# Performance work log

Hardware: AMD Instinct MI355X
Metric: run time of the kernel (lower is better)

## Reference

```python
import jax, jax.numpy as jnp
import numpy as np

HIDDEN = 1024
VOCAB = 128000

def setup_inputs() -> dict:
    key = jax.random.key(0)
    ks = jax.random.split(key, 9)
    s = 0.02
    return {
        "seq_input": jax.random.randint(ks[0], (1,), 0, VOCAB),
        "hidden": jax.random.normal(ks[1], (1, 1, HIDDEN), dtype=jnp.float32),
        "emb": jax.random.normal(ks[2], (VOCAB, HIDDEN), dtype=jnp.float32) * s,
        "w_ih": jax.random.normal(ks[3], (3 * HIDDEN, HIDDEN), dtype=jnp.float32) * s,
        "w_hh": jax.random.normal(ks[4], (3 * HIDDEN, HIDDEN), dtype=jnp.float32) * s,
        "b_ih": jax.random.normal(ks[5], (3 * HIDDEN,), dtype=jnp.float32) * s,
        "b_hh": jax.random.normal(ks[6], (3 * HIDDEN,), dtype=jnp.float32) * s,
        "w_out": jax.random.normal(ks[7], (VOCAB, HIDDEN), dtype=jnp.float32) * s,
        "b_out": jax.random.normal(ks[8], (VOCAB,), dtype=jnp.float32) * s,
    }

def reference(seq_input, hidden, emb, w_ih, w_hh, b_ih, b_hh, w_out, b_out):
    # embedding lookup + relu: [1, H]
    x = jax.nn.relu(emb[seq_input])
    h = hidden[0]  # [1, H] (num_layers=1, batch=1)
    # single-step GRU (PyTorch gate ordering: r, z, n)
    gi = x @ w_ih.T + b_ih     # [1, 3H]
    gh = h @ w_hh.T + b_hh     # [1, 3H]
    i_r, i_z, i_n = jnp.split(gi, 3, axis=-1)
    h_r, h_z, h_n = jnp.split(gh, 3, axis=-1)
    r = jax.nn.sigmoid(i_r + h_r)
    z = jax.nn.sigmoid(i_z + h_z)
    n = jnp.tanh(i_n + r * h_n)
    h_new = (1.0 - z) * n + z * h  # [1, H]
    # output projection + log-softmax over vocab: [1, V]
    logits = h_new @ w_out.T + b_out
    logprobs = jax.nn.log_softmax(logits, axis=1)
    return logprobs, h_new[None]  # hidden back to [1,1,H]
```

## Files before the change

### kernel.cpp

```cpp
#include <hip/hip_runtime.h>

#define H 1024
#define V 128000

#define WS_GI   0
#define WS_GH   3072
#define WS_HN   6144
#define WS_PART 7168
#define WS_FIN  7424

__device__ __forceinline__ float wave_sum(float acc) {
    #pragma unroll
    for (int m = 32; m >= 1; m >>= 1) acc += __shfl_xor(acc, m);
    return acc;
}

__global__ void gates_kernel(const int* __restrict__ seq,
                             const float* __restrict__ hidden,
                             const float* __restrict__ emb,
                             const float* __restrict__ w_ih,
                             const float* __restrict__ w_hh,
                             const float* __restrict__ b_ih,
                             const float* __restrict__ b_hh,
                             float* __restrict__ ws) {
    const int wid  = threadIdx.x >> 6;
    const int lane = threadIdx.x & 63;
    const int row  = blockIdx.x * 4 + wid;
    if (row >= 6144) return;
    const int idx = seq[0];

    const float* wrow;
    const float* v;
    float bias;
    bool relu_in;
    if (row < 3072) {
        wrow = w_ih + (size_t)row * H;
        v    = emb + (size_t)idx * H;
        bias = b_ih[row];
        relu_in = true;
    } else {
        const int r = row - 3072;
        wrow = w_hh + (size_t)r * H;
        v    = hidden;
        bias = b_hh[r];
        relu_in = false;
    }

    float acc = 0.f;
    #pragma unroll
    for (int k = 0; k < 4; ++k) {
        const int j = lane * 4 + k * 256;
        float4 wv = *(const float4*)(wrow + j);
        float4 vv = *(const float4*)(v + j);
        if (relu_in) {
            vv.x = fmaxf(vv.x, 0.f); vv.y = fmaxf(vv.y, 0.f);
            vv.z = fmaxf(vv.z, 0.f); vv.w = fmaxf(vv.w, 0.f);
        }
        acc += wv.x * vv.x + wv.y * vv.y + wv.z * vv.z + wv.w * vv.w;
    }
    acc = wave_sum(acc);
    if (lane == 0) ws[row] = acc + bias;
}

__global__ void gru_kernel(const float* __restrict__ hidden,
                           float* __restrict__ ws,
                           float* __restrict__ out) {
    const int i = threadIdx.x;
    const float gi_r = ws[WS_GI + i];
    const float gi_z = ws[WS_GI + H + i];
    const float gi_n = ws[WS_GI + 2 * H + i];
    const float gh_r = ws[WS_GH + i];
    const float gh_z = ws[WS_GH + H + i];
    const float gh_n = ws[WS_GH + 2 * H + i];
    const float r = 1.f / (1.f + expf(-(gi_r + gh_r)));
    const float z = 1.f / (1.f + expf(-(gi_z + gh_z)));
    const float n = tanhf(gi_n + r * gh_n);
    const float h = hidden[i];
    const float hn = (1.f - z) * n + z * h;
    ws[WS_HN + i] = hn;
    out[V + i] = hn;
}

__global__ void logits_kernel(const float* __restrict__ w_out,
                              const float* __restrict__ b_out,
                              const float* __restrict__ ws,
                              float* __restrict__ out) {
    const int wid  = threadIdx.x >> 6;
    const int lane = threadIdx.x & 63;
    const float* h = ws + WS_HN;
    float4 hv[4];
    #pragma unroll
    for (int k = 0; k < 4; ++k) hv[k] = *(const float4*)(h + lane * 4 + k * 256);

    const int nwaves = gridDim.x * 4;
    for (int row = blockIdx.x * 4 + wid; row < V; row += nwaves) {
        const float* wr = w_out + (size_t)row * H;
        float acc = 0.f;
        #pragma unroll
        for (int k = 0; k < 4; ++k) {
            float4 wv = *(const float4*)(wr + lane * 4 + k * 256);
            acc += wv.x * hv[k].x + wv.y * hv[k].y + wv.z * hv[k].z + wv.w * hv[k].w;
        }
        acc = wave_sum(acc);
        if (lane == 0) out[row] = acc + b_out[row];
    }
}

__device__ __forceinline__ void online_combine(float& m, float& s, float om, float os) {
    const float M = fmaxf(m, om);
    s = s * expf(m - M) + os * expf(om - M);
    m = M;
}

__global__ void smax_partial(const float* __restrict__ out, float* __restrict__ ws) {
    const int base = blockIdx.x * 1024 + threadIdx.x;
    float m = -1e30f, s = 0.f;
    #pragma unroll
    for (int k = 0; k < 4; ++k) {
        const float x = out[base + k * 256];
        if (x > m) { s = s * expf(m - x) + 1.f; m = x; }
        else       { s += expf(x - m); }
    }
    #pragma unroll
    for (int d = 1; d < 64; d <<= 1) {
        const float om = __shfl_xor(m, d);
        const float os = __shfl_xor(s, d);
        online_combine(m, s, om, os);
    }
    __shared__ float sm[4], sss[4];
    const int wid  = threadIdx.x >> 6;
    const int lane = threadIdx.x & 63;
    if (lane == 0) { sm[wid] = m; sss[wid] = s; }
    __syncthreads();
    if (threadIdx.x == 0) {
        float M = sm[0], S = sss[0];
        #pragma unroll
        for (int w = 1; w < 4; ++w) online_combine(M, S, sm[w], sss[w]);
        ws[WS_PART + 2 * blockIdx.x]     = M;
        ws[WS_PART + 2 * blockIdx.x + 1] = S;
    }
}

__global__ void smax_final(float* __restrict__ ws) {
    const int lane = threadIdx.x;
    float m = -1e30f, s = 0.f;
    for (int i = lane; i < 125; i += 64) {
        online_combine(m, s, ws[WS_PART + 2 * i], ws[WS_PART + 2 * i + 1]);
    }
    #pragma unroll
    for (int d = 1; d < 64; d <<= 1) {
        const float om = __shfl_xor(m, d);
        const float os = __shfl_xor(s, d);
        online_combine(m, s, om, os);
    }
    if (lane == 0) { ws[WS_FIN] = m; ws[WS_FIN + 1] = logf(s); }
}

__global__ void smax_write(float* __restrict__ out, const float* __restrict__ ws) {
    const float c = ws[WS_FIN] + ws[WS_FIN + 1];
    const int i = (blockIdx.x * 256 + threadIdx.x) * 4;
    float4 v = *(float4*)(out + i);
    v.x -= c; v.y -= c; v.z -= c; v.w -= c;
    *(float4*)(out + i) = v;
}

extern "C" void kernel_launch(void* const* d_in, const int* in_sizes, int n_in,
                              void* d_out, int out_size, void* d_ws, size_t ws_size,
                              hipStream_t stream) {
    const int*   seq    = (const int*)d_in[0];
    const float* hidden = (const float*)d_in[1];
    const float* emb    = (const float*)d_in[2];
    const float* w_ih   = (const float*)d_in[3];
    const float* w_hh   = (const float*)d_in[4];
    const float* b_ih   = (const float*)d_in[5];
    const float* b_hh   = (const float*)d_in[6];
    const float* w_out  = (const float*)d_in[7];
    const float* b_out  = (const float*)d_in[8];
    float* out = (float*)d_out;
    float* ws  = (float*)d_ws;

    gates_kernel<<<1536, 256, 0, stream>>>(seq, hidden, emb, w_ih, w_hh, b_ih, b_hh, ws);
    gru_kernel<<<1, 1024, 0, stream>>>(hidden, ws, out);
    logits_kernel<<<2000, 256, 0, stream>>>(w_out, b_out, ws, out);
    smax_partial<<<125, 256, 0, stream>>>(out, ws);
    smax_final<<<1, 64, 0, stream>>>(ws);
    smax_write<<<125, 256, 0, stream>>>(out, ws);
}
```

Before: 115.7 us.

## Fuse GRU cell and softmax partials into logits kernel, cut launches to three

Each logits block now recomputes the GRU cell update redundantly into shared memory, replacing the single-block gru kernel. The online max/sum-exp is accumulated inside the logits loop, which removes the separate partial-reduction pass over the logits. The final reduction over 2000 partials is folded into each block of the write kernel. This removes three launches and one read of the vocab-sized logits, at the cost of redundant gate work per block and each write block re-reducing all 2000 partials.

Measured after the change: 111.6 us. 1.04x faster.

```diff
diff --git a/kernel.cpp b/kernel.cpp
--- a/kernel.cpp
+++ b/kernel.cpp
@@ -2,17 +2,22 @@
 
 #define H 1024
 #define V 128000
+#define NBLK_LOGITS 2000
 
 #define WS_GI   0
 #define WS_GH   3072
-#define WS_HN   6144
-#define WS_PART 7168
-#define WS_FIN  7424
+#define WS_PART 6144
 
 __device__ __forceinline__ float wave_sum(float acc) {
     #pragma unroll
     for (int m = 32; m >= 1; m >>= 1) acc += __shfl_xor(acc, m);
     return acc;
+}
+
+__device__ __forceinline__ void online_combine(float& m, float& s, float om, float os) {
+    const float M = fmaxf(m, om);
+    s = s * expf(m - M) + os * expf(om - M);
+    m = M;
 }
 
 __global__ void gates_kernel(const int* __restrict__ seq,
@@ -62,37 +67,49 @@
     if (lane == 0) ws[row] = acc + bias;
 }
 
-__global__ void gru_kernel(const float* __restrict__ hidden,
-                           float* __restrict__ ws,
-                           float* __restrict__ out) {
-    const int i = threadIdx.x;
-    const float gi_r = ws[WS_GI + i];
-    const float gi_z = ws[WS_GI + H + i];
-    const float gi_n = ws[WS_GI + 2 * H + i];
-    const float gh_r = ws[WS_GH + i];
-    const float gh_z = ws[WS_GH + H + i];
-    const float gh_n = ws[WS_GH + 2 * H + i];
-    const float r = 1.f / (1.f + expf(-(gi_r + gh_r)));
-    const float z = 1.f / (1.f + expf(-(gi_z + gh_z)));
-    const float n = tanhf(gi_n + r * gh_n);
-    const float h = hidden[i];
-    const float hn = (1.f - z) * n + z * h;
-    ws[WS_HN + i] = hn;
-    out[V + i] = hn;
-}
+__global__ void __launch_bounds__(256) logits_kernel(
+        const float* __restrict__ hidden,
+        const float* __restrict__ w_out,
+        const float* __restrict__ b_out,
+        float* __restrict__ ws,
+        float* __restrict__ out) {
+    __shared__ float sh_h[H];
+    __shared__ float sm[4], ssum[4];
+    const int tid = threadIdx.x;
 
-__global__ void logits_kernel(const float* __restrict__ w_out,
-                              const float* __restrict__ b_out,
-                              const float* __restrict__ ws,
-                              float* __restrict__ out) {
-    const int wid  = threadIdx.x >> 6;
-    const int lane = threadIdx.x & 63;
-    const float* h = ws + WS_HN;
+    #pragma unroll
+    for (int k = 0; k < 4; ++k) {
+        const int i = tid + k * 256;
+        const float gi_r = ws[WS_GI + i];
+        const float gi_z = ws[WS_GI + H + i];
+        const float gi_n = ws[WS_GI + 2 * H + i];
+        const float gh_r = ws[WS_GH + i];
+        const float gh_z = ws[WS_GH + H + i];
+        const float gh_n = ws[WS_GH + 2 * H + i];
+        const float r = 1.f / (1.f + expf(-(gi_r + gh_r)));
+        const float z = 1.f / (1.f + expf(-(gi_z + gh_z)));
+        const float n = tanhf(gi_n + r * gh_n);
+        const float h = hidden[i];
+        sh_h[i] = (1.f - z) * n + z * h;
+    }
+    __syncthreads();
+
+    if (blockIdx.x == 0) {
+        #pragma unroll
+        for (int k = 0; k < 4; ++k) {
+            const int i = tid + k * 256;
+            out[V + i] = sh_h[i];
+        }
+    }
+
+    const int wid  = tid >> 6;
+    const int lane = tid & 63;
     float4 hv[4];
     #pragma unroll
-    for (int k = 0; k < 4; ++k) hv[k] = *(const float4*)(h + lane * 4 + k * 256);
+    for (int k = 0; k < 4; ++k) hv[k] = *(const float4*)(&sh_h[lane * 4 + k * 256]);
 
-    const int nwaves = gridDim.x * 4;
+    float m = -1e30f, s = 0.f;
+    const int nwaves = NBLK_LOGITS * 4;
     for (int row = blockIdx.x * 4 + wid; row < V; row += nwaves) {
         const float* wr = w_out + (size_t)row * H;
         float acc = 0.f;
@@ -101,50 +118,32 @@
             float4 wv = *(const float4*)(wr + lane * 4 + k * 256);
             acc += wv.x * hv[k].x + wv.y * hv[k].y + wv.z * hv[k].z + wv.w * hv[k].w;
         }
-        acc = wave_sum(acc);
-        if (lane == 0) out[row] = acc + b_out[row];
+        acc = wave_sum(acc) + b_out[row];
+        if (lane == 0) out[row] = acc;
+        if (acc > m) { s = s * expf(m - acc) + 1.f; m = acc; }
+        else         { s += expf(acc - m); }
     }
-}
 
-__device__ __forceinline__ void online_combine(float& m, float& s, float om, float os) {
-    const float M = fmaxf(m, om);
-    s = s * expf(m - M) + os * expf(om - M);
-    m = M;
-}
-
-__global__ void smax_partial(const float* __restrict__ out, float* __restrict__ ws) {
-    const int base = blockIdx.x * 1024 + threadIdx.x;
-    float m = -1e30f, s = 0.f;
-    #pragma unroll
-    for (int k = 0; k < 4; ++k) {
-        const float x = out[base + k * 256];
-        if (x > m) { s = s * expf(m - x) + 1.f; m = x; }
-        else       { s += expf(x - m); }
-    }
-    #pragma unroll
-    for (int d = 1; d < 64; d <<= 1) {
-        const float om = __shfl_xor(m, d);
-        const float os = __shfl_xor(s, d);
-        online_combine(m, s, om, os);
-    }
-    __shared__ float sm[4], sss[4];
-    const int wid  = threadIdx.x >> 6;
-    const int lane = threadIdx.x & 63;
-    if (lane == 0) { sm[wid] = m; sss[wid] = s; }
+    if (lane == 0) { sm[wid] = m; ssum[wid] = s; }
     __syncthreads();
-    if (threadIdx.x == 0) {
-        float M = sm[0], S = sss[0];
+    if (tid == 0) {
+        float M = sm[0], S = ssum[0];
         #pragma unroll
-        for (int w = 1; w < 4; ++w) online_combine(M, S, sm[w], sss[w]);
+        for (int w = 1; w < 4; ++w) online_combine(M, S, sm[w], ssum[w]);
         ws[WS_PART + 2 * blockIdx.x]     = M;
         ws[WS_PART + 2 * blockIdx.x + 1] = S;
     }
 }
 
-__global__ void smax_final(float* __restrict__ ws) {
-    const int lane = threadIdx.x;
+__global__ void smax_write(float* __restrict__ out, const float* __restrict__ ws) {
+    const int tid  = threadIdx.x;
+    const int wid  = tid >> 6;
+    const int lane = tid & 63;
+    __shared__ float sm[4], ssum[4];
+    __shared__ float c_sh;
+
     float m = -1e30f, s = 0.f;
-    for (int i = lane; i < 125; i += 64) {
+    for (int i = tid; i < NBLK_LOGITS; i += 256) {
         online_combine(m, s, ws[WS_PART + 2 * i], ws[WS_PART + 2 * i + 1]);
     }
     #pragma unroll
@@ -153,12 +152,18 @@
         const float os = __shfl_xor(s, d);
         online_combine(m, s, om, os);
     }
-    if (lane == 0) { ws[WS_FIN] = m; ws[WS_FIN + 1] = logf(s); }
-}
+    if (lane == 0) { sm[wid] = m; ssum[wid] = s; }
+    __syncthreads();
+    if (tid == 0) {
+        float M = sm[0], S = ssum[0];
+        #pragma unroll
+        for (int w = 1; w < 4; ++w) online_combine(M, S, sm[w], ssum[w]);
+        c_sh = M + logf(S);
+    }
+    __syncthreads();
+    const float c = c_sh;
 
-__global__ void smax_write(float* __restrict__ out, const float* __restrict__ ws) {
-    const float c = ws[WS_FIN] + ws[WS_FIN + 1];
-    const int i = (blockIdx.x * 256 + threadIdx.x) * 4;
+    const int i = (blockIdx.x * 256 + tid) * 4;
     float4 v = *(float4*)(out + i);
     v.x -= c; v.y -= c; v.z -= c; v.w -= c;
     *(float4*)(out + i) = v;
@@ -180,9 +185,6 @@
     float* ws  = (float*)d_ws;
 
     gates_kernel<<<1536, 256, 0, stream>>>(seq, hidden, emb, w_ih, w_hh, b_ih, b_hh, ws);
-    gru_kernel<<<1, 1024, 0, stream>>>(hidden, ws, out);
-    logits_kernel<<<2000, 256, 0, stream>>>(w_out, b_out, ws, out);
-    smax_partial<<<125, 256, 0, stream>>>(out, ws);
-    smax_final<<<1, 64, 0, stream>>>(ws);
+    logits_kernel<<<NBLK_LOGITS, 256, 0, stream>>>(hidden, w_out, b_out, ws, out);
     smax_write<<<125, 256, 0, stream>>>(out, ws);
 }
```
